# Performance work log

Hardware: AMD Instinct MI355X
Metric: run time of the kernel (lower is better)

Reference implementation:

```python
import jax, jax.numpy as jnp
import numpy as np

T, H = 8192, 2048


def setup_inputs() -> dict:
    key = jax.random.key(0)
    k1, k2, k3 = jax.random.split(key, 3)
    x_sequence = jax.random.normal(k1, (T, H), dtype=jnp.float32)
    lamda = jax.random.normal(k2, (H,), dtype=jnp.float32) * 0.2
    B = jax.random.normal(k3, (H, H), dtype=jnp.float32) / np.sqrt(H).astype(np.float32)
    return {"x_sequence": x_sequence, "lamda": lamda, "B": B}


def reference(x_sequence, lamda, B):
    # Batched input projection: u_t = B @ x_t for all t -> one GEMM. [T, H]
    u = x_sequence @ B.T
    # Linear diagonal recurrence h_t = lamda * h_{t-1} + u_t with h_0 = 0,
    # solved with a log-depth associative scan over (a, b) pairs where
    # combine((a1,b1),(a2,b2)) = (a2*a1, a2*b1 + b2).
    a = jnp.broadcast_to(lamda, u.shape)  # [T, H]

    def combine(c1, c2):
        a1, b1 = c1
        a2, b2 = c2
        return (a2 * a1, a2 * b1 + b2)

    _, h = jax.lax.associative_scan(combine, (a, u))
    return h  # [T, H] stacked hidden states
```

## Files before the change

kernel.cpp:

```cpp
#include <hip/hip_runtime.h>
#include <hip/hip_bf16.h>


#define TDIM 8192
#define HDIM 2048
#define BM 128
#define BN 256
#define BK 32
#define NIT (HDIM / BK)
#define ASLOT 4096
#define BSLOT 8192
#define LCH 64
#define GCH (TDIM / LCH)

#define BBF_BYTES (HDIM * HDIM * 2)
#define E_BYTES   (GCH * HDIM * 4)
#define WS_NEED   ((size_t)BBF_BYTES + E_BYTES)

typedef float f32x4 __attribute__((ext_vector_type(4)));
typedef short s16x4 __attribute__((ext_vector_type(4)));
typedef short s16x8 __attribute__((ext_vector_type(8)));

static __device__ __forceinline__ short f2bf(float f) {
  __bf16 b = (__bf16)f;
  return __builtin_bit_cast(short, b);
}

#define GL(gp, lp)                                                            \
  __builtin_amdgcn_global_load_lds(                                           \
      (const __attribute__((address_space(1))) void*)(gp),                    \
      (__attribute__((address_space(3))) void*)(lp), 16, 0, 0)

__global__ void cvt_B(const float* __restrict__ src, short* __restrict__ dst) {
  const int base = blockIdx.x * 1024;
  const int t = threadIdx.x;
  f32x4 v0 = *(const f32x4*)(src + (size_t)(base +   0 + t) * 4);
  f32x4 v1 = *(const f32x4*)(src + (size_t)(base + 256 + t) * 4);
  f32x4 v2 = *(const f32x4*)(src + (size_t)(base + 512 + t) * 4);
  f32x4 v3 = *(const f32x4*)(src + (size_t)(base + 768 + t) * 4);
#define STORE1(v_, off_) do {                                                 \
    s16x4 o;                                                                  \
    o[0] = f2bf(v_[0]); o[1] = f2bf(v_[1]);                                   \
    o[2] = f2bf(v_[2]); o[3] = f2bf(v_[3]);                                   \
    *(s16x4*)(dst + (size_t)(base + (off_) + t) * 4) = o;                     \
  } while (0)
  STORE1(v0, 0); STORE1(v1, 256); STORE1(v2, 512); STORE1(v3, 768);
#undef STORE1
}

__global__ __launch_bounds__(256, 2) void gemm_hyb2(
    const float* __restrict__ X, const short* __restrict__ Bb,
    const float* __restrict__ lam,
    float* __restrict__ U, float* __restrict__ e) {
  __shared__ __align__(16) short As[2][ASLOT];
  __shared__ __align__(16) short Bs[2][BSLOT];

  const int wg  = blockIdx.x;
  const int swz = (wg & 7) * 64 + (wg >> 3);
  const int tm = swz >> 3;
  const int tn = swz & 7;
  const int row0 = tm * BM, col0 = tn * BN;

  const int tid  = threadIdx.x;
  const int lane = tid & 63;
  const int wid  = tid >> 6;
  const int wr = (wid >> 1) * 64;
  const int wc = (wid & 1) * 128;
  const int r16 = lane & 15;
  const int g4  = lane >> 4;

  int offA[4], offB[8];
#pragma unroll
  for (int m = 0; m < 4; ++m) {
    const int r = wr + m * 16 + r16;
    offA[m] = r * 32 + ((g4 ^ ((r >> 1) & 3)) << 3);
  }
#pragma unroll
  for (int n = 0; n < 8; ++n) {
    const int r = wc + n * 16 + r16;
    offB[n] = r * 32 + ((g4 ^ ((r >> 1) & 3)) << 3);
  }

  const float* gA = X + (size_t)(row0 + (tid >> 3)) * HDIM + (tid & 7) * 4;
  const int offWbase = (((((tid & 7) >> 1) ^ ((tid >> 4) & 3)) << 3) + (tid & 1) * 4)
                       + (tid >> 3) * 32;

  const int sgB = (tid & 3) ^ ((tid >> 3) & 3);
  const short* gB = Bb + (size_t)(col0 + (tid >> 2)) * HDIM + sgB * 8;

#define ISSUE_A(dst, t_) do {                                                 \
    _Pragma("unroll") for (int c = 0; c < 4; ++c)                             \
      dst[c] = *(const f32x4*)(gA + (size_t)c * 32 * HDIM + (t_) * BK);       \
  } while (0)

#define CVTWR_A(arr, sl) do {                                                 \
    _Pragma("unroll") for (int c = 0; c < 4; ++c) {                           \
      s16x4 v;                                                                \
      v[0] = f2bf(arr[c][0]); v[1] = f2bf(arr[c][1]);                         \
      v[2] = f2bf(arr[c][2]); v[3] = f2bf(arr[c][3]);                         \
      *(s16x4*)&As[sl][offWbase + c * 32 * 32] = v;                           \
    }                                                                         \
  } while (0)

#define GLOADB(sl, t_) do {                                                   \
    _Pragma("unroll") for (int c = 0; c < 4; ++c)                             \
      GL(gB + (size_t)c * 64 * HDIM + (t_) * BK,                              \
         &Bs[sl][(c * 256 + tid) * 8]);                                       \
  } while (0)

#define PHASE(sl) do {                                                        \
    s16x8 af[4], bfv[8];                                                      \
    _Pragma("unroll") for (int m = 0; m < 4; ++m)                             \
      af[m] = *(const s16x8*)&As[sl][offA[m]];                                \
    _Pragma("unroll") for (int n = 0; n < 8; ++n)                             \
      bfv[n] = *(const s16x8*)&Bs[sl][offB[n]];                               \
    __builtin_amdgcn_s_setprio(1);                                            \
    _Pragma("unroll") for (int m = 0; m < 4; ++m)                             \
      _Pragma("unroll") for (int n = 0; n < 8; ++n)                           \
        acc[m][n] = __builtin_amdgcn_mfma_f32_16x16x32_bf16(                  \
            af[m], bfv[n], acc[m][n], 0, 0, 0);                               \
    __builtin_amdgcn_s_setprio(0);                                            \
  } while (0)

  f32x4 acc[4][8] = {};
  f32x4 ra[4];

  ISSUE_A(ra, 0);
  GLOADB(0, 0);
  CVTWR_A(ra, 0);
  __syncthreads();

#pragma unroll 2
  for (int j = 0; j < NIT - 1; ++j) {
    const int cur = j & 1;
    ISSUE_A(ra, j + 1);
    GLOADB(cur ^ 1, j + 1);
    PHASE(cur);
    CVTWR_A(ra, cur ^ 1);
    __syncthreads();
  }
  PHASE((NIT - 1) & 1);

  const int crow = row0 + wr + (g4 << 2);
  const int ccol = col0 + wc + r16;
#pragma unroll
  for (int m = 0; m < 4; ++m)
#pragma unroll
    for (int n = 0; n < 8; ++n)
#pragma unroll
      for (int j = 0; j < 4; ++j)
        U[(size_t)(crow + m * 16 + j) * HDIM + ccol + n * 16] = acc[m][n][j];

#pragma unroll
  for (int n = 0; n < 8; ++n) {
    const int c = ccol + n * 16;
    const float l  = lam[c];
    const float l2 = l * l;
    const float l4 = l2 * l2;
    const float l8 = l4 * l4;
    const float l16 = l8 * l8;
    float lg = 1.f;
    if (g4 < 3) lg = l4;
    if (g4 < 2) lg *= l4;
    if (g4 < 1) lg *= l4;
    float S = 0.f;
#pragma unroll
    for (int m = 0; m < 4; ++m) {
      const f32x4 a = acc[m][n];
      const float T = ((a[0] * l + a[1]) * l + a[2]) * l + a[3];
      S = S * l16 + T;
    }
    S *= lg;
    S += __shfl_xor(S, 16, 64);
    S += __shfl_xor(S, 32, 64);
    if (g4 == 0) {
      const int j = tm * 2 + (wid >> 1);
      e[(size_t)j * HDIM + c] = S;
    }
  }

#undef ISSUE_A
#undef CVTWR_A
#undef GLOADB
#undef PHASE
}

__global__ void pass3f(float* __restrict__ U, const float* __restrict__ lam,
                       const float* __restrict__ e) {
  const int c = (blockIdx.y * 256 + threadIdx.x) * 4;
  const int j = blockIdx.x;
  const f32x4 l4 = *(const f32x4*)&lam[c];
  f32x4 p = l4;
#pragma unroll
  for (int i = 0; i < 6; ++i) p = p * p;
  f32x4 E = {0.f, 0.f, 0.f, 0.f};
  for (int jp = 0; jp < j; ++jp) {
    f32x4 ej = *(const f32x4*)&e[(size_t)jp * HDIM + c];
    E = p * E + ej;
  }
  float* up = U + (size_t)j * LCH * HDIM + c;
  f32x4 h = E;
#pragma unroll 4
  for (int t = 0; t < LCH; ++t) {
    f32x4 u4 = *(const f32x4*)up;
    h = l4 * h + u4;
    *(f32x4*)up = h;
    up += HDIM;
  }
}

__global__ __launch_bounds__(256, 2) void gemm_f32_fb(
    const float* __restrict__ X, const float* __restrict__ Bm,
    float* __restrict__ U) {
#define LDK 40
#define FBM 128
#define FBK 32
#define FNT (HDIM / FBK)
  __shared__ __align__(16) short As[2][FBM * LDK];
  __shared__ __align__(16) short Bs[2][FBM * LDK];
  const int wg  = blockIdx.x;
  const int cpx = (TDIM / FBM) * (HDIM / FBM) / 8;
  const int swz = (wg & 7) * cpx + (wg >> 3);
  const int tm = swz >> 4;
  const int tn = swz & 15;
  const int row0 = tm * FBM, col0 = tn * FBM;
  const int tid  = threadIdx.x;
  const int lane = tid & 63;
  const int wid  = tid >> 6;
  const int wr = (wid >> 1) * 64;
  const int wc = (wid & 1) * 64;
  const int srow = tid >> 2;
  const int sk   = (tid & 3) << 3;
  const float* gA  = X  + (size_t)(row0 + srow) * HDIM + sk;
  const float* gA2 = gA + 64 * HDIM;
  const float* gB  = Bm + (size_t)(col0 + srow) * HDIM + sk;
  const float* gB2 = gB + 64 * HDIM;
  f32x4 a00, a01, a10, a11, b00, b01, b10, b11;
#define LOADREG(kt) do {                                                      \
    const float* p;                                                           \
    p = gA  + (kt) * FBK; a00 = *(const f32x4*)p; a01 = *(const f32x4*)(p+4); \
    p = gA2 + (kt) * FBK; a10 = *(const f32x4*)p; a11 = *(const f32x4*)(p+4); \
    p = gB  + (kt) * FBK; b00 = *(const f32x4*)p; b01 = *(const f32x4*)(p+4); \
    p = gB2 + (kt) * FBK; b10 = *(const f32x4*)p; b11 = *(const f32x4*)(p+4); \
  } while (0)
#define CVT8(v, lo, hi) do {                                                  \
    v[0] = f2bf(lo[0]); v[1] = f2bf(lo[1]); v[2] = f2bf(lo[2]);               \
    v[3] = f2bf(lo[3]); v[4] = f2bf(hi[0]); v[5] = f2bf(hi[1]);               \
    v[6] = f2bf(hi[2]); v[7] = f2bf(hi[3]);                                   \
  } while (0)
#define DSWRITE(buf) do {                                                     \
    s16x8 v;                                                                  \
    CVT8(v, a00, a01); *(s16x8*)&As[buf][srow * LDK + sk] = v;                \
    CVT8(v, a10, a11); *(s16x8*)&As[buf][(srow + 64) * LDK + sk] = v;         \
    CVT8(v, b00, b01); *(s16x8*)&Bs[buf][srow * LDK + sk] = v;                \
    CVT8(v, b10, b11); *(s16x8*)&Bs[buf][(srow + 64) * LDK + sk] = v;         \
  } while (0)
  f32x4 acc[4][4] = {};
#define COMPUTE(buf) do {                                                     \
    const int r16_ = lane & 15;                                               \
    const int ks_  = (lane >> 4) * 8;                                         \
    s16x8 af[4], bfr[4];                                                      \
    _Pragma("unroll") for (int m = 0; m < 4; ++m)                             \
      af[m] = *(const s16x8*)&As[buf][(wr + m * 16 + r16_) * LDK + ks_];      \
    _Pragma("unroll") for (int n = 0; n < 4; ++n)                             \
      bfr[n] = *(const s16x8*)&Bs[buf][(wc + n * 16 + r16_) * LDK + ks_];     \
    _Pragma("unroll") for (int m = 0; m < 4; ++m)                             \
      _Pragma("unroll") for (int n = 0; n < 4; ++n)                           \
        acc[m][n] = __builtin_amdgcn_mfma_f32_16x16x32_bf16(                  \
            af[m], bfr[n], acc[m][n], 0, 0, 0);                               \
  } while (0)
  LOADREG(0);
  DSWRITE(0);
  __syncthreads();
#pragma unroll 2
  for (int kt = 0; kt < FNT; ++kt) {
    const int cur = kt & 1;
    if (kt + 1 < FNT) LOADREG(kt + 1);
    COMPUTE(cur);
    if (kt + 1 < FNT) DSWRITE(cur ^ 1);
    __syncthreads();
  }
  const int crow = wr + ((lane >> 4) << 2);
  const int ccol = wc + (lane & 15);
#pragma unroll
  for (int m = 0; m < 4; ++m)
#pragma unroll
    for (int n = 0; n < 4; ++n)
#pragma unroll
      for (int j = 0; j < 4; ++j)
        U[(size_t)(row0 + crow + m * 16 + j) * HDIM + (col0 + ccol + n * 16)] =
            acc[m][n][j];
#undef LOADREG
#undef CVT8
#undef DSWRITE
#undef COMPUTE
#undef LDK
#undef FBM
#undef FBK
#undef FNT
}

__global__ void scan_pass1(const float* __restrict__ U,
                           const float* __restrict__ lam,
                           float* __restrict__ e) {
  const int c = (blockIdx.y * 256 + threadIdx.x) * 4;
  const int j = blockIdx.x;
  const f32x4 l4 = *(const f32x4*)&lam[c];
  f32x4 h = {0.f, 0.f, 0.f, 0.f};
  const float* up = U + (size_t)j * LCH * HDIM + c;
#pragma unroll 4
  for (int t = 0; t < LCH; ++t) {
    f32x4 u4 = *(const f32x4*)up;
    h = l4 * h + u4;
    up += HDIM;
  }
  *(f32x4*)&e[(size_t)j * HDIM + c] = h;
}

extern "C" void kernel_launch(void* const* d_in, const int* in_sizes, int n_in,
                              void* d_out, int out_size, void* d_ws, size_t ws_size,
                              hipStream_t stream) {
  const float* X   = (const float*)d_in[0];
  const float* lam = (const float*)d_in[1];
  const float* Bm  = (const float*)d_in[2];
  float* U = (float*)d_out;

  if (ws_size >= WS_NEED) {
    short* Bb = (short*)d_ws;
    float* e  = (float*)((char*)d_ws + BBF_BYTES);

    cvt_B<<<dim3(HDIM * HDIM / 4096), dim3(256), 0, stream>>>(Bm, Bb);
    gemm_hyb2<<<dim3((TDIM / BM) * (HDIM / BN)), dim3(256), 0, stream>>>(
        X, Bb, lam, U, e);
    pass3f<<<dim3(GCH, HDIM / 1024), dim3(256), 0, stream>>>(U, lam, e);
  } else {
    float* e = (float*)d_ws;
    gemm_f32_fb<<<dim3((TDIM / 128) * (HDIM / 128)), dim3(256), 0, stream>>>(
        X, Bm, U);
    scan_pass1<<<dim3(GCH, HDIM / 1024), dim3(256), 0, stream>>>(U, lam, e);
    pass3f<<<dim3(GCH, HDIM / 1024), dim3(256), 0, stream>>>(U, lam, e);
  }
}
```

Before: 127.0 us.

## Fuse B bf16 conversion into GEMM and move to 512-thread workgroups

Drops the separate B fp32-to-bf16 conversion kernel and its workspace buffer. The GEMM now loads fp32 B tiles directly through registers, converts them in-kernel and writes them to LDS, replacing the direct global-to-LDS loads of pre-converted bf16 B. The workgroup grows to 512 threads in 8 waves with a 64x64 tile per wave, and A/B staging is simplified to one 8-element row chunk per thread. This saves a launch and the round trip of B through memory, but each workgroup now reads B at twice the byte width and spends extra VALU on conversion, with B re-read by all 64 row tiles.

```diff
diff --git a/kernel.cpp b/kernel.cpp
--- a/kernel.cpp
+++ b/kernel.cpp
@@ -8,17 +8,10 @@
 #define BN 256
 #define BK 32
 #define NIT (HDIM / BK)
-#define ASLOT 4096
-#define BSLOT 8192
 #define LCH 64
 #define GCH (TDIM / LCH)
 
-#define BBF_BYTES (HDIM * HDIM * 2)
-#define E_BYTES   (GCH * HDIM * 4)
-#define WS_NEED   ((size_t)BBF_BYTES + E_BYTES)
-
 typedef float f32x4 __attribute__((ext_vector_type(4)));
-typedef short s16x4 __attribute__((ext_vector_type(4)));
 typedef short s16x8 __attribute__((ext_vector_type(8)));
 
 static __device__ __forceinline__ short f2bf(float f) {
@@ -26,34 +19,12 @@
   return __builtin_bit_cast(short, b);
 }
 
-#define GL(gp, lp)                                                            \
-  __builtin_amdgcn_global_load_lds(                                           \
-      (const __attribute__((address_space(1))) void*)(gp),                    \
-      (__attribute__((address_space(3))) void*)(lp), 16, 0, 0)
-
-__global__ void cvt_B(const float* __restrict__ src, short* __restrict__ dst) {
-  const int base = blockIdx.x * 1024;
-  const int t = threadIdx.x;
-  f32x4 v0 = *(const f32x4*)(src + (size_t)(base +   0 + t) * 4);
-  f32x4 v1 = *(const f32x4*)(src + (size_t)(base + 256 + t) * 4);
-  f32x4 v2 = *(const f32x4*)(src + (size_t)(base + 512 + t) * 4);
-  f32x4 v3 = *(const f32x4*)(src + (size_t)(base + 768 + t) * 4);
-#define STORE1(v_, off_) do {                                                 \
-    s16x4 o;                                                                  \
-    o[0] = f2bf(v_[0]); o[1] = f2bf(v_[1]);                                   \
-    o[2] = f2bf(v_[2]); o[3] = f2bf(v_[3]);                                   \
-    *(s16x4*)(dst + (size_t)(base + (off_) + t) * 4) = o;                     \
-  } while (0)
-  STORE1(v0, 0); STORE1(v1, 256); STORE1(v2, 512); STORE1(v3, 768);
-#undef STORE1
-}
-
-__global__ __launch_bounds__(256, 2) void gemm_hyb2(
-    const float* __restrict__ X, const short* __restrict__ Bb,
+__global__ __launch_bounds__(512, 4) void gemm_hyb3(
+    const float* __restrict__ X, const float* __restrict__ Bm,
     const float* __restrict__ lam,
     float* __restrict__ U, float* __restrict__ e) {
-  __shared__ __align__(16) short As[2][ASLOT];
-  __shared__ __align__(16) short Bs[2][BSLOT];
+  __shared__ __align__(16) short As[2][BM * BK];
+  __shared__ __align__(16) short Bs[2][BN * BK];
 
   const int wg  = blockIdx.x;
   const int swz = (wg & 7) * 64 + (wg >> 3);
@@ -64,79 +35,91 @@
   const int tid  = threadIdx.x;
   const int lane = tid & 63;
   const int wid  = tid >> 6;
-  const int wr = (wid >> 1) * 64;
-  const int wc = (wid & 1) * 128;
+  const int wr = (wid >> 2) * 64;
+  const int wc = (wid & 3) * 64;
   const int r16 = lane & 15;
   const int g4  = lane >> 4;
 
-  int offA[4], offB[8];
+  int offA[4], offB[4];
 #pragma unroll
   for (int m = 0; m < 4; ++m) {
     const int r = wr + m * 16 + r16;
     offA[m] = r * 32 + ((g4 ^ ((r >> 1) & 3)) << 3);
   }
 #pragma unroll
-  for (int n = 0; n < 8; ++n) {
+  for (int n = 0; n < 4; ++n) {
     const int r = wc + n * 16 + r16;
     offB[n] = r * 32 + ((g4 ^ ((r >> 1) & 3)) << 3);
   }
 
-  const float* gA = X + (size_t)(row0 + (tid >> 3)) * HDIM + (tid & 7) * 4;
-  const int offWbase = (((((tid & 7) >> 1) ^ ((tid >> 4) & 3)) << 3) + (tid & 1) * 4)
-                       + (tid >> 3) * 32;
-
-  const int sgB = (tid & 3) ^ ((tid >> 3) & 3);
-  const short* gB = Bb + (size_t)(col0 + (tid >> 2)) * HDIM + sgB * 8;
-
-#define ISSUE_A(dst, t_) do {                                                 \
-    _Pragma("unroll") for (int c = 0; c < 4; ++c)                             \
-      dst[c] = *(const f32x4*)(gA + (size_t)c * 32 * HDIM + (t_) * BK);       \
-  } while (0)
-
-#define CVTWR_A(arr, sl) do {                                                 \
-    _Pragma("unroll") for (int c = 0; c < 4; ++c) {                           \
-      s16x4 v;                                                                \
-      v[0] = f2bf(arr[c][0]); v[1] = f2bf(arr[c][1]);                         \
-      v[2] = f2bf(arr[c][2]); v[3] = f2bf(arr[c][3]);                         \
-      *(s16x4*)&As[sl][offWbase + c * 32 * 32] = v;                           \
+  const int gl = (tid & 3) ^ ((tid >> 3) & 3);
+  const float* gA = X  + (size_t)(row0 + (tid >> 2)) * HDIM + gl * 8;
+  const float* gB = Bm + (size_t)(col0 + (tid >> 2)) * HDIM + gl * 8;
+
+#define ISSUE_A(t_) do {                                                      \
+    ra[0] = *(const f32x4*)(gA + (t_) * BK);                                  \
+    ra[1] = *(const f32x4*)(gA + (t_) * BK + 4);                              \
+  } while (0)
+
+#define ISSUE_B(t_) do {                                                      \
+    _Pragma("unroll") for (int c = 0; c < 2; ++c) {                           \
+      const float* p = gB + (size_t)c * 128 * HDIM + (t_) * BK;               \
+      rb[2 * c]     = *(const f32x4*)p;                                       \
+      rb[2 * c + 1] = *(const f32x4*)(p + 4);                                 \
     }                                                                         \
   } while (0)
 
-#define GLOADB(sl, t_) do {                                                   \
-    _Pragma("unroll") for (int c = 0; c < 4; ++c)                             \
-      GL(gB + (size_t)c * 64 * HDIM + (t_) * BK,                              \
-         &Bs[sl][(c * 256 + tid) * 8]);                                       \
+#define CVTWR_A(sl) do {                                                      \
+    s16x8 v;                                                                  \
+    v[0] = f2bf(ra[0][0]); v[1] = f2bf(ra[0][1]);                             \
+    v[2] = f2bf(ra[0][2]); v[3] = f2bf(ra[0][3]);                             \
+    v[4] = f2bf(ra[1][0]); v[5] = f2bf(ra[1][1]);                             \
+    v[6] = f2bf(ra[1][2]); v[7] = f2bf(ra[1][3]);                             \
+    *(s16x8*)&As[sl][tid * 8] = v;                                            \
+  } while (0)
+
+#define CVTWR_B(sl) do {                                                      \
+    _Pragma("unroll") for (int c = 0; c < 2; ++c) {                           \
+      s16x8 v;                                                                \
+      v[0] = f2bf(rb[2*c][0]); v[1] = f2bf(rb[2*c][1]);                       \
+      v[2] = f2bf(rb[2*c][2]); v[3] = f2bf(rb[2*c][3]);                       \
+      v[4] = f2bf(rb[2*c+1][0]); v[5] = f2bf(rb[2*c+1][1]);                   \
+      v[6] = f2bf(rb[2*c+1][2]); v[7] = f2bf(rb[2*c+1][3]);                   \
+      *(s16x8*)&Bs[sl][(c * 512 + tid) * 8] = v;                              \
+    }                                                                         \
   } while (0)
 
 #define PHASE(sl) do {                                                        \
-    s16x8 af[4], bfv[8];                                                      \
+    s16x8 af[4], bfv[4];                                                      \
     _Pragma("unroll") for (int m = 0; m < 4; ++m)                             \
       af[m] = *(const s16x8*)&As[sl][offA[m]];                                \
-    _Pragma("unroll") for (int n = 0; n < 8; ++n)                             \
+    _Pragma("unroll") for (int n = 0; n < 4; ++n)                             \
       bfv[n] = *(const s16x8*)&Bs[sl][offB[n]];                               \
     __builtin_amdgcn_s_setprio(1);                                            \
     _Pragma("unroll") for (int m = 0; m < 4; ++m)                             \
-      _Pragma("unroll") for (int n = 0; n < 8; ++n)                           \
+      _Pragma("unroll") for (int n = 0; n < 4; ++n)                           \
         acc[m][n] = __builtin_amdgcn_mfma_f32_16x16x32_bf16(                  \
             af[m], bfv[n], acc[m][n], 0, 0, 0);                               \
     __builtin_amdgcn_s_setprio(0);                                            \
   } while (0)
 
-  f32x4 acc[4][8] = {};
-  f32x4 ra[4];
-
-  ISSUE_A(ra, 0);
-  GLOADB(0, 0);
-  CVTWR_A(ra, 0);
+  f32x4 acc[4][4] = {};
+  f32x4 ra[2], rb[4];
+
+  ISSUE_A(0);
+  ISSUE_B(0);
+  CVTWR_A(0);
+  CVTWR_B(0);
   __syncthreads();
 
 #pragma unroll 2
   for (int j = 0; j < NIT - 1; ++j) {
     const int cur = j & 1;
-    ISSUE_A(ra, j + 1);
-    GLOADB(cur ^ 1, j + 1);
+    ISSUE_A(j + 1);
+    ISSUE_B(j + 1);
     PHASE(cur);
-    CVTWR_A(ra, cur ^ 1);
+    CVTWR_A(cur ^ 1);
+    CVTWR_B(cur ^ 1);
     __syncthreads();
   }
   PHASE((NIT - 1) & 1);
@@ -146,13 +129,13 @@
 #pragma unroll
   for (int m = 0; m < 4; ++m)
 #pragma unroll
-    for (int n = 0; n < 8; ++n)
+    for (int n = 0; n < 4; ++n)
 #pragma unroll
       for (int j = 0; j < 4; ++j)
         U[(size_t)(crow + m * 16 + j) * HDIM + ccol + n * 16] = acc[m][n][j];
 
 #pragma unroll
-  for (int n = 0; n < 8; ++n) {
+  for (int n = 0; n < 4; ++n) {
     const int c = ccol + n * 16;
     const float l  = lam[c];
     const float l2 = l * l;
@@ -174,14 +157,15 @@
     S += __shfl_xor(S, 16, 64);
     S += __shfl_xor(S, 32, 64);
     if (g4 == 0) {
-      const int j = tm * 2 + (wid >> 1);
+      const int j = tm * 2 + (wid >> 2);
       e[(size_t)j * HDIM + c] = S;
     }
   }
 
 #undef ISSUE_A
+#undef ISSUE_B
 #undef CVTWR_A
-#undef GLOADB
+#undef CVTWR_B
 #undef PHASE
 }
 
@@ -324,17 +308,13 @@
   const float* lam = (const float*)d_in[1];
   const float* Bm  = (const float*)d_in[2];
   float* U = (float*)d_out;
-
-  if (ws_size >= WS_NEED) {
-    short* Bb = (short*)d_ws;
-    float* e  = (float*)((char*)d_ws + BBF_BYTES);
-
-    cvt_B<<<dim3(HDIM * HDIM / 4096), dim3(256), 0, stream>>>(Bm, Bb);
-    gemm_hyb2<<<dim3((TDIM / BM) * (HDIM / BN)), dim3(256), 0, stream>>>(
-        X, Bb, lam, U, e);
+  float* e = (float*)d_ws;
+
+  if (ws_size >= (size_t)GCH * HDIM * 4) {
+    gemm_hyb3<<<dim3((TDIM / BM) * (HDIM / BN)), dim3(512), 0, stream>>>(
+        X, Bm, lam, U, e);
     pass3f<<<dim3(GCH, HDIM / 1024), dim3(256), 0, stream>>>(U, lam, e);
   } else {
-    float* e = (float*)d_ws;
     gemm_f32_fb<<<dim3((TDIM / 128) * (HDIM / 128)), dim3(256), 0, stream>>>(
         X, Bm, U);
     scan_pass1<<<dim3(GCH, HDIM / 1024), dim3(256), 0, stream>>>(U, lam, e);
```

New measurement: 217.6 us. 1.71x slower.
